# Performance work log

Measured on AMD Instinct MI355X. Metric: run time of the kernel, lower is better.

The kernel has to match this reference:

```python
import jax, jax.numpy as jnp
import numpy as np

N, C, L, D, F = 8, 128, 512, 64, 512
ATTN_W = 64
LN_EPS = 1e-5
ATTN_EPS = 1e-6


def _xavier(k, shape):
    lim = float(np.sqrt(6.0 / (shape[0] + shape[1])))
    return jax.random.uniform(k, shape, jnp.float32, -lim, lim)


def setup_inputs() -> dict:
    key = jax.random.key(0)
    ks = jax.random.split(key, 8)
    return dict(
        x=jax.random.normal(ks[0], (N, C, L), jnp.float32),
        Wx=_xavier(ks[1], (C, D)),
        Wt=_xavier(ks[2], (C, D)),
        bh=jnp.zeros((D,), jnp.float32),
        Wa=_xavier(ks[3], (D, 1)),
        ba=jnp.zeros((1,), jnp.float32),
        W0=_xavier(ks[4], (C, F)),
        b0=jnp.zeros((F,), jnp.float32),
        W1=_xavier(ks[5], (F, C)),
        b1=jnp.zeros((C,), jnp.float32),
        g0=jnp.ones((C,), jnp.float32),
        be0=jnp.zeros((C,), jnp.float32),
        g1=jnp.ones((C,), jnp.float32),
        be1=jnp.zeros((C,), jnp.float32),
    )


def _layernorm(y, g, b):
    mu = jnp.mean(y, axis=-1, keepdims=True)
    var = jnp.var(y, axis=-1, keepdims=True)
    return (y - mu) * jax.lax.rsqrt(var + LN_EPS) * g + b


def reference(x, Wx, Wt, bh, Wa, ba, W0, b0, W1, b1, g0, be0, g1, be1):
    xt = jnp.transpose(x, (0, 2, 1))  # (N, L, C)
    q = jnp.einsum('nlc,cd->nld', xt, Wt)  # (N, L, D)
    k = jnp.einsum('nlc,cd->nld', xt, Wx)  # (N, L, D)
    # additive (Bahdanau) scores: h is the large (N, L, L, D) intermediate
    h = jnp.tanh(q[:, :, None, :] + k[:, None, :, :] + bh)
    e = jnp.einsum('nlmd,d->nlm', h, Wa[:, 0]) + ba[0]  # (N, L, L)
    e = jnp.exp(e - jnp.max(e, axis=-1, keepdims=True))
    # local band mask: tril(w//2 - 1) & triu(-w//2) on (row i, col j)
    dij = jnp.arange(L)[None, :] - jnp.arange(L)[:, None]  # j - i
    mask = (dij <= ATTN_W // 2 - 1) & (dij >= -(ATTN_W // 2))
    e = jnp.where(mask, e, 0.0)
    a = e / (jnp.sum(e, axis=-1, keepdims=True) + ATTN_EPS)  # (N, L, L)
    v = jnp.einsum('nlm,nmc->nlc', a, xt)  # (N, L, C)
    x2 = _layernorm(v + xt, g0, be0)
    x3 = jnp.einsum('nlf,fc->nlc', jax.nn.relu(jnp.einsum('nlc,cf->nlf', x2, W0) + b0), W1) + b1
    x4 = _layernorm(x3 + x2, g1, be1)
    return (jnp.transpose(x4, (0, 2, 1)), a)
```

## Files before the change

### kernel.cpp

```cpp
#include <hip/hip_runtime.h>
#include <hip/hip_fp16.h>
#include <cstddef>


__global__ __launch_bounds__(512) void prep_kernel(
    const float* __restrict__ x, const float* __restrict__ Wt,
    const float* __restrict__ Wx, float* __restrict__ q,
    float* __restrict__ k) {
  __shared__ float xs[128][17];
  int tid = threadIdx.x;
  int n = blockIdx.x >> 5;
  int l0 = (blockIdx.x & 31) << 4;

  {
    int c = tid >> 2, v = tid & 3;
    float4 d4 = *(const float4*)(x + ((size_t)n * 128 + c) * 512 + l0 + 4 * v);
    xs[c][4 * v + 0] = d4.x; xs[c][4 * v + 1] = d4.y;
    xs[c][4 * v + 2] = d4.z; xs[c][4 * v + 3] = d4.w;
  }
  __syncthreads();

  int half = tid >> 8;
  int t = tid & 255;
  int r = t >> 4;
  int f0 = (t & 15) << 2;
  const float* W = half ? Wx : Wt;
  float* dst = half ? k : q;
  float acc[4] = {0.f, 0.f, 0.f, 0.f};
#pragma unroll 4
  for (int cc = 0; cc < 128; cc++) {
    float xv = xs[cc][r];
    float4 w = *(const float4*)(W + cc * 64 + f0);
    acc[0] += xv * w.x; acc[1] += xv * w.y;
    acc[2] += xv * w.z; acc[3] += xv * w.w;
  }
  *(float4*)(dst + ((size_t)n * 512 + l0 + r) * 64 + f0) =
      make_float4(acc[0], acc[1], acc[2], acc[3]);
}

__global__ __launch_bounds__(512, 4) void attn_ffn_fused_kernel(
    const float* __restrict__ x, const float* __restrict__ q,
    const float* __restrict__ k, const float* __restrict__ bh,
    const float* __restrict__ Wa, const float* __restrict__ ba,
    const float* __restrict__ g0, const float* __restrict__ be0,
    const float* __restrict__ W0, const float* __restrict__ b0,
    const float* __restrict__ W1, const float* __restrict__ b1,
    const float* __restrict__ g1, const float* __restrict__ be1,
    float* __restrict__ a, float* __restrict__ out) {
  __shared__ __align__(16) char smem[41328];
  __shared__ __align__(16) float xstT[128][12];
  __shared__ __align__(16) float avT[72][12];
  __shared__ float was[64];

  float (*ks)[68] = (float(*)[68])smem;
  float (*qs)[64] = (float(*)[64])(smem + 19312);
  __half* xtw = (__half*)(smem + 21360);
  float (*partB)[8][128] = (float(*)[8][128])smem;
  float (*tstT)[12] = (float(*)[12])smem;
  float (*part)[8][128] = (float(*)[8][128])smem;

  int tid = threadIdx.x;
  int w = tid >> 6, lane = tid & 63;
  int bid = blockIdx.x;
  int tile = (bid & 7) * 64 + (bid >> 3);
  size_t rbase = (size_t)tile * 8;
  int n = (int)(rbase >> 9);
  int i0 = (int)(rbase & 511);
  int jlo0 = i0 - 32;

  if (tid < 64) was[tid] = Wa[tid];
  for (int idx = tid; idx < 72 * 12; idx += 512) ((float*)avT)[idx] = 0.f;
  if (tid < 128) {
    int r = tid >> 4, d4 = (tid & 15) << 2;
    float4 qv = *(const float4*)(q + ((size_t)n * 512 + i0 + r) * 64 + d4);
    float4 bv = *(const float4*)(bh + d4);
    *(float4*)(&qs[r][d4]) =
        make_float4(qv.x + bv.x, qv.y + bv.y, qv.z + bv.z, qv.w + bv.w);
  }
  for (int idx = tid; idx < 71 * 16; idx += 512) {
    int row = idx >> 4, d4 = (idx & 15) << 2;
    int j = jlo0 + row;
    float4 v = make_float4(0.f, 0.f, 0.f, 0.f);
    if (j >= 0 && j < 512)
      v = *(const float4*)(k + ((size_t)n * 512 + j) * 64 + d4);
    *(float4*)(&ks[row][d4]) = v;
  }
  for (int t = tid; t < 128 * 18; t += 512) {
    int c = t / 18;
    int u = t - c * 18;
    int col = 4 * u;
    int j0 = jlo0 + col;
    const float* xp = x + ((size_t)n * 128 + c) * 512;
    float4 v = make_float4(0.f, 0.f, 0.f, 0.f);
    if (j0 >= 0 && j0 + 3 < 512) {
      v = *(const float4*)(xp + j0);
    } else {
      if (j0 + 0 >= 0 && j0 + 0 < 512) v.x = xp[j0 + 0];
      if (j0 + 1 >= 0 && j0 + 1 < 512) v.y = xp[j0 + 1];
      if (j0 + 2 >= 0 && j0 + 2 < 512) v.z = xp[j0 + 2];
      if (j0 + 3 >= 0 && j0 + 3 < 512) v.w = xp[j0 + 3];
    }
    __half2 p01, p23;
    p01.x = __float2half(v.x); p01.y = __float2half(v.y);
    p23.x = __float2half(v.z); p23.y = __float2half(v.w);
    *(__half2*)(xtw + c * 78 + col) = p01;
    *(__half2*)(xtw + c * 78 + col + 2) = p23;
  }
  __syncthreads();

  {
    int r = w;
    int i = i0 + r;
    int j = jlo0 + r + lane;
    bool valid = (j >= 0 && j < 512);
    const float* krow = &ks[r + lane][0];
    float e = 0.f;
#pragma unroll
    for (int d4 = 0; d4 < 64; d4 += 4) {
      float4 kv = *(const float4*)(krow + d4);
      float4 qv = *(const float4*)(&qs[r][d4]);
      float4 wv = *(const float4*)(&was[d4]);
      float h0 = qv.x + kv.x, h1 = qv.y + kv.y;
      float h2 = qv.z + kv.z, h3 = qv.w + kv.w;
      float t0 = 1.f - 2.f * __builtin_amdgcn_rcpf(__expf(2.f * h0) + 1.f);
      float t1 = 1.f - 2.f * __builtin_amdgcn_rcpf(__expf(2.f * h1) + 1.f);
      float t2 = 1.f - 2.f * __builtin_amdgcn_rcpf(__expf(2.f * h2) + 1.f);
      float t3 = 1.f - 2.f * __builtin_amdgcn_rcpf(__expf(2.f * h3) + 1.f);
      e += wv.x * t0 + wv.y * t1 + wv.z * t2 + wv.w * t3;
    }
    e += ba[0];
    if (!valid) e = -1e30f;

    float m = e;
    for (int o = 32; o > 0; o >>= 1) m = fmaxf(m, __shfl_xor(m, o, 64));
    float ex = valid ? __expf(e - m) : 0.f;
    float s = ex;
    for (int o = 32; o > 0; o >>= 1) s += __shfl_xor(s, o, 64);
    avT[r + lane][r] = ex / (s + 1e-6f);

    float* arow = a + ((size_t)n * 512 + i) * 512;
    int jlo = i - 32;
#pragma unroll
    for (int t = 0; t < 2; t++) {
      int col0 = 4 * lane + 256 * t;
      float4 v;
      { int jr = col0 + 0 - jlo; int jc = min(max(jr, 0), 63); v.x = (jr >= 0 && jr < 64) ? avT[r + jc][r] : 0.f; }
      { int jr = col0 + 1 - jlo; int jc = min(max(jr, 0), 63); v.y = (jr >= 0 && jr < 64) ? avT[r + jc][r] : 0.f; }
      { int jr = col0 + 2 - jlo; int jc = min(max(jr, 0), 63); v.z = (jr >= 0 && jr < 64) ? avT[r + jc][r] : 0.f; }
      { int jr = col0 + 3 - jlo; int jc = min(max(jr, 0), 63); v.w = (jr >= 0 && jr < 64) ? avT[r + jc][r] : 0.f; }
      *(float4*)(arow + col0) = v;
    }
  }
  __syncthreads();

  {
    int c = tid & 127;
    int g = tid >> 7;
    const __half* xr = xtw + c * 78;
    float acc[8] = {0.f, 0.f, 0.f, 0.f, 0.f, 0.f, 0.f, 0.f};
    int colb = 18 * g;
#pragma unroll
    for (int u = 0; u < 9; u++) {
      int col = colb + 2 * u;
      __half2 xh = *(const __half2*)(xr + col);
      float xv0 = __half2float(__low2half(xh));
      float xv1 = __half2float(__high2half(xh));
      float4 a0lo = *(const float4*)(&avT[col][0]);
      float4 a0hi = *(const float4*)(&avT[col][4]);
      float4 a1lo = *(const float4*)(&avT[col + 1][0]);
      float4 a1hi = *(const float4*)(&avT[col + 1][4]);
      acc[0] += a0lo.x * xv0 + a1lo.x * xv1;
      acc[1] += a0lo.y * xv0 + a1lo.y * xv1;
      acc[2] += a0lo.z * xv0 + a1lo.z * xv1;
      acc[3] += a0lo.w * xv0 + a1lo.w * xv1;
      acc[4] += a0hi.x * xv0 + a1hi.x * xv1;
      acc[5] += a0hi.y * xv0 + a1hi.y * xv1;
      acc[6] += a0hi.z * xv0 + a1hi.z * xv1;
      acc[7] += a0hi.w * xv0 + a1hi.w * xv1;
    }
#pragma unroll
    for (int r = 0; r < 8; r++) partB[g][r][c] = acc[r];
  }
  __syncthreads();

  {
    int c = tid & 127;
    int r = tid >> 7;
    const float* xp = x + ((size_t)n * 128 + c) * 512;
    float s0 = partB[0][r][c] + partB[1][r][c] + partB[2][r][c] + partB[3][r][c];
    float s1 = partB[0][r + 4][c] + partB[1][r + 4][c] +
               partB[2][r + 4][c] + partB[3][r + 4][c];
    xstT[c][r] = s0 + xp[i0 + r];
    xstT[c][r + 4] = s1 + xp[i0 + r + 4];
  }
  __syncthreads();

  {
    float a0 = xstT[lane][w], a1 = xstT[lane + 64][w];
    float s = a0 + a1, s2 = a0 * a0 + a1 * a1;
    for (int o = 32; o > 0; o >>= 1) {
      s += __shfl_xor(s, o, 64);
      s2 += __shfl_xor(s2, o, 64);
    }
    float mu = s * (1.f / 128.f);
    float var = s2 * (1.f / 128.f) - mu * mu;
    float rs = rsqrtf(var + 1e-5f);
    xstT[lane][w] = (a0 - mu) * rs * g0[lane] + be0[lane];
    xstT[lane + 64][w] = (a1 - mu) * rs * g0[lane + 64] + be0[lane + 64];
  }
  __syncthreads();

  {
    int g = lane & 15;
    int kq = lane >> 4;
    int f0 = (16 * w + g) << 2;
    int ccb = kq << 5;
    const float* w0p = W0 + (size_t)ccb * 512 + f0;
    float acc[8][4];
#pragma unroll
    for (int i = 0; i < 8; i++)
#pragma unroll
      for (int u = 0; u < 4; u++) acc[i][u] = 0.f;

    float4 wbuf[4];
#pragma unroll
    for (int p = 0; p < 4; p++)
      wbuf[p] = *(const float4*)(w0p + (size_t)p * 512);
#pragma unroll
    for (int c4 = 0; c4 < 8; c4++) {
      float4 cur0 = wbuf[0], cur1 = wbuf[1], cur2 = wbuf[2], cur3 = wbuf[3];
      if (c4 < 7) {
#pragma unroll
        for (int p = 0; p < 4; p++)
          wbuf[p] = *(const float4*)(w0p + (size_t)((c4 + 1) * 4 + p) * 512);
      }
#pragma unroll
      for (int p = 0; p < 4; p++) {
        int cc = ccb + c4 * 4 + p;
        float4 wv = (p == 0) ? cur0 : (p == 1) ? cur1 : (p == 2) ? cur2 : cur3;
        float4 xa = *(const float4*)(&xstT[cc][0]);
        float4 xb = *(const float4*)(&xstT[cc][4]);
        acc[0][0] += xa.x * wv.x; acc[0][1] += xa.x * wv.y; acc[0][2] += xa.x * wv.z; acc[0][3] += xa.x * wv.w;
        acc[1][0] += xa.y * wv.x; acc[1][1] += xa.y * wv.y; acc[1][2] += xa.y * wv.z; acc[1][3] += xa.y * wv.w;
        acc[2][0] += xa.z * wv.x; acc[2][1] += xa.z * wv.y; acc[2][2] += xa.z * wv.z; acc[2][3] += xa.z * wv.w;
        acc[3][0] += xa.w * wv.x; acc[3][1] += xa.w * wv.y; acc[3][2] += xa.w * wv.z; acc[3][3] += xa.w * wv.w;
        acc[4][0] += xb.x * wv.x; acc[4][1] += xb.x * wv.y; acc[4][2] += xb.x * wv.z; acc[4][3] += xb.x * wv.w;
        acc[5][0] += xb.y * wv.x; acc[5][1] += xb.y * wv.y; acc[5][2] += xb.y * wv.z; acc[5][3] += xb.y * wv.w;
        acc[6][0] += xb.z * wv.x; acc[6][1] += xb.z * wv.y; acc[6][2] += xb.z * wv.z; acc[6][3] += xb.z * wv.w;
        acc[7][0] += xb.w * wv.x; acc[7][1] += xb.w * wv.y; acc[7][2] += xb.w * wv.z; acc[7][3] += xb.w * wv.w;
      }
    }
#pragma unroll
    for (int i = 0; i < 8; i++)
#pragma unroll
      for (int u = 0; u < 4; u++) {
        float v = acc[i][u];
        v += __shfl_xor(v, 16, 64);
        v += __shfl_xor(v, 32, 64);
        acc[i][u] = v;
      }
    int f = f0 + kq;
    float bb = b0[f];
    float r0v[8];
#pragma unroll
    for (int i = 0; i < 8; i++) {
      float v = (kq == 0) ? acc[i][0] : (kq == 1) ? acc[i][1]
              : (kq == 2) ? acc[i][2] : acc[i][3];
      r0v[i] = fmaxf(v + bb, 0.f);
    }
    *(float4*)(&tstT[f][0]) = make_float4(r0v[0], r0v[1], r0v[2], r0v[3]);
    *(float4*)(&tstT[f][4]) = make_float4(r0v[4], r0v[5], r0v[6], r0v[7]);
  }
  __syncthreads();

  float g2acc[4][4];
  {
    int c0 = (lane & 31) << 2;
    int rh = lane >> 5;
    const float* W1p = W1 + (size_t)w * 64 * 128 + c0;
    int tb = w << 6;
#pragma unroll
    for (int i = 0; i < 4; i++)
#pragma unroll
      for (int u = 0; u < 4; u++) g2acc[i][u] = 0.f;

    float4 wbuf[4];
#pragma unroll
    for (int p = 0; p < 4; p++)
      wbuf[p] = *(const float4*)(W1p + (size_t)p * 128);
#pragma unroll
    for (int t4 = 0; t4 < 16; t4++) {
      float4 cur0 = wbuf[0], cur1 = wbuf[1], cur2 = wbuf[2], cur3 = wbuf[3];
      if (t4 < 15) {
#pragma unroll
        for (int p = 0; p < 4; p++)
          wbuf[p] = *(const float4*)(W1p + (size_t)((t4 + 1) * 4 + p) * 128);
      }
#pragma unroll
      for (int p = 0; p < 4; p++) {
        int t = t4 * 4 + p;
        float4 wv = (p == 0) ? cur0 : (p == 1) ? cur1 : (p == 2) ? cur2 : cur3;
        float4 tv = *(const float4*)(&tstT[tb + t][4 * rh]);
        g2acc[0][0] += tv.x * wv.x; g2acc[0][1] += tv.x * wv.y; g2acc[0][2] += tv.x * wv.z; g2acc[0][3] += tv.x * wv.w;
        g2acc[1][0] += tv.y * wv.x; g2acc[1][1] += tv.y * wv.y; g2acc[1][2] += tv.y * wv.z; g2acc[1][3] += tv.y * wv.w;
        g2acc[2][0] += tv.z * wv.x; g2acc[2][1] += tv.z * wv.y; g2acc[2][2] += tv.z * wv.z; g2acc[2][3] += tv.z * wv.w;
        g2acc[3][0] += tv.w * wv.x; g2acc[3][1] += tv.w * wv.y; g2acc[3][2] += tv.w * wv.z; g2acc[3][3] += tv.w * wv.w;
      }
    }
  }
  __syncthreads();

  {
    int c0 = (lane & 31) << 2;
    int rh = lane >> 5;
#pragma unroll
    for (int i = 0; i < 4; i++) {
      *(float4*)(&part[w][4 * rh + i][c0]) =
          make_float4(g2acc[i][0], g2acc[i][1], g2acc[i][2], g2acc[i][3]);
    }
  }
  __syncthreads();

  {
    float a0 = b1[lane] + xstT[lane][w];
    float a1 = b1[lane + 64] + xstT[lane + 64][w];
#pragma unroll
    for (int ko = 0; ko < 8; ko++) {
      a0 += part[ko][w][lane];
      a1 += part[ko][w][lane + 64];
    }
    float s = a0 + a1, s2 = a0 * a0 + a1 * a1;
    for (int o = 32; o > 0; o >>= 1) {
      s += __shfl_xor(s, o, 64);
      s2 += __shfl_xor(s2, o, 64);
    }
    float mu = s * (1.f / 128.f);
    float var = s2 * (1.f / 128.f) - mu * mu;
    float rs = rsqrtf(var + 1e-5f);
    xstT[lane][w] = (a0 - mu) * rs * g1[lane] + be1[lane];
    xstT[lane + 64][w] = (a1 - mu) * rs * g1[lane + 64] + be1[lane + 64];
  }
  __syncthreads();

  {
    int c = tid >> 2, tq = tid & 3;
    *(float2*)(out + ((size_t)n * 128 + c) * 512 + i0 + 2 * tq) =
        make_float2(xstT[c][2 * tq], xstT[c][2 * tq + 1]);
  }
}

extern "C" void kernel_launch(void* const* d_in, const int* in_sizes, int n_in,
                              void* d_out, int out_size, void* d_ws, size_t ws_size,
                              hipStream_t stream) {
  const float* x   = (const float*)d_in[0];
  const float* Wx  = (const float*)d_in[1];
  const float* Wt  = (const float*)d_in[2];
  const float* bh  = (const float*)d_in[3];
  const float* Wa  = (const float*)d_in[4];
  const float* ba  = (const float*)d_in[5];
  const float* W0  = (const float*)d_in[6];
  const float* b0  = (const float*)d_in[7];
  const float* W1  = (const float*)d_in[8];
  const float* b1  = (const float*)d_in[9];
  const float* g0  = (const float*)d_in[10];
  const float* be0 = (const float*)d_in[11];
  const float* g1  = (const float*)d_in[12];
  const float* be1 = (const float*)d_in[13];

  float* outx = (float*)d_out;
  float* outa = outx + (size_t)524288;

  float* ws = (float*)d_ws;
  float* q  = ws;
  float* k  = q + 262144;

  prep_kernel<<<256, 512, 0, stream>>>(x, Wt, Wx, q, k);
  attn_ffn_fused_kernel<<<512, 512, 0, stream>>>(
      x, q, k, bh, Wa, ba, g0, be0, W0, b0, W1, b1, g1, be1, outa, outx);
}
```

Baseline: 122.1 us.

## Run FFN matmuls on fp16 MFMA with pre-packed half-precision weights

New measurement: 110.3 us. 1.11x faster.

```diff
diff --git a/kernel.cpp b/kernel.cpp
--- a/kernel.cpp
+++ b/kernel.cpp
@@ -3,10 +3,15 @@
 #include <cstddef>
 
 
+typedef _Float16 half8_t __attribute__((ext_vector_type(8)));
+typedef float f32x4_t __attribute__((ext_vector_type(4)));
+
 __global__ __launch_bounds__(512) void prep_kernel(
     const float* __restrict__ x, const float* __restrict__ Wt,
-    const float* __restrict__ Wx, float* __restrict__ q,
-    float* __restrict__ k) {
+    const float* __restrict__ Wx, const float* __restrict__ W0,
+    const float* __restrict__ W1, float* __restrict__ q,
+    float* __restrict__ k, _Float16* __restrict__ W0p,
+    _Float16* __restrict__ W1p) {
   __shared__ float xs[128][17];
   int tid = threadIdx.x;
   int n = blockIdx.x >> 5;
@@ -36,6 +41,27 @@
   }
   *(float4*)(dst + ((size_t)n * 512 + l0 + r) * 64 + f0) =
       make_float4(acc[0], acc[1], acc[2], acc[3]);
+
+  if (tid < 64) {
+    int b = blockIdx.x;
+    int l15 = tid & 15, lk = tid >> 4;
+    if (b < 128) {
+      int ft = b >> 2, ks = b & 3;
+      const float* src = W0 + (size_t)(ks * 32 + lk * 8) * 512 + ft * 16 + l15;
+      half8_t v;
+#pragma unroll
+      for (int j = 0; j < 8; j++) v[j] = (_Float16)src[(size_t)j * 512];
+      *(half8_t*)(W0p + (size_t)b * 512 + tid * 8) = v;
+    } else {
+      int tt = b - 128;
+      int ft = tt >> 4, ks = tt & 15;
+      const float* src = W1 + (size_t)(ks * 32 + lk * 8) * 128 + ft * 16 + l15;
+      half8_t v;
+#pragma unroll
+      for (int j = 0; j < 8; j++) v[j] = (_Float16)src[(size_t)j * 128];
+      *(half8_t*)(W1p + (size_t)tt * 512 + tid * 8) = v;
+    }
+  }
 }
 
 __global__ __launch_bounds__(512, 4) void attn_ffn_fused_kernel(
@@ -43,8 +69,8 @@
     const float* __restrict__ k, const float* __restrict__ bh,
     const float* __restrict__ Wa, const float* __restrict__ ba,
     const float* __restrict__ g0, const float* __restrict__ be0,
-    const float* __restrict__ W0, const float* __restrict__ b0,
-    const float* __restrict__ W1, const float* __restrict__ b1,
+    const _Float16* __restrict__ W0p, const float* __restrict__ b0,
+    const _Float16* __restrict__ W1p, const float* __restrict__ b1,
     const float* __restrict__ g1, const float* __restrict__ be1,
     float* __restrict__ a, float* __restrict__ out) {
   __shared__ __align__(16) char smem[41328];
@@ -56,8 +82,9 @@
   float (*qs)[64] = (float(*)[64])(smem + 19312);
   __half* xtw = (__half*)(smem + 21360);
   float (*partB)[8][128] = (float(*)[8][128])smem;
-  float (*tstT)[12] = (float(*)[12])smem;
-  float (*part)[8][128] = (float(*)[8][128])smem;
+  _Float16* x2h = (_Float16*)smem;
+  _Float16* tsth = (_Float16*)(smem + 4352);
+  float (*ys)[128] = (float(*)[128])(smem + 20992);
 
   int tid = threadIdx.x;
   int w = tid >> 6, lane = tid & 63;
@@ -211,124 +238,66 @@
   __syncthreads();
 
   {
-    int g = lane & 15;
-    int kq = lane >> 4;
-    int f0 = (16 * w + g) << 2;
-    int ccb = kq << 5;
-    const float* w0p = W0 + (size_t)ccb * 512 + f0;
-    float acc[8][4];
-#pragma unroll
-    for (int i = 0; i < 8; i++)
-#pragma unroll
-      for (int u = 0; u < 4; u++) acc[i][u] = 0.f;
-
-    float4 wbuf[4];
-#pragma unroll
-    for (int p = 0; p < 4; p++)
-      wbuf[p] = *(const float4*)(w0p + (size_t)p * 512);
-#pragma unroll
-    for (int c4 = 0; c4 < 8; c4++) {
-      float4 cur0 = wbuf[0], cur1 = wbuf[1], cur2 = wbuf[2], cur3 = wbuf[3];
-      if (c4 < 7) {
-#pragma unroll
-        for (int p = 0; p < 4; p++)
-          wbuf[p] = *(const float4*)(w0p + (size_t)((c4 + 1) * 4 + p) * 512);
+    half8_t z = {};
+    half8_t* xpad = (half8_t*)(x2h + 8 * 136);
+    for (int idx = tid; idx < 136; idx += 512) xpad[idx] = z;
+    half8_t* tpad = (half8_t*)(tsth + 8 * 520);
+    for (int idx = tid; idx < 520; idx += 512) tpad[idx] = z;
+    int c = tid & 127, rr = tid >> 7;
+    x2h[rr * 136 + c] = (_Float16)xstT[c][rr];
+    x2h[(rr + 4) * 136 + c] = (_Float16)xstT[c][rr + 4];
+  }
+  __syncthreads();
+
+  {
+    int l15 = lane & 15, lk = lane >> 4;
+    const _Float16* arow = x2h + l15 * 136;
+    half8_t afrag[4];
+#pragma unroll
+    for (int ksi = 0; ksi < 4; ksi++)
+      afrag[ksi] = *(const half8_t*)(arow + ksi * 32 + lk * 8);
+#pragma unroll
+    for (int i = 0; i < 4; i++) {
+      int ft = 4 * w + i;
+      f32x4_t acc = {0.f, 0.f, 0.f, 0.f};
+#pragma unroll
+      for (int ksi = 0; ksi < 4; ksi++) {
+        half8_t b = *(const half8_t*)(W0p + ((size_t)(ft * 4 + ksi) << 9) + lane * 8);
+        acc = __builtin_amdgcn_mfma_f32_16x16x32_f16(afrag[ksi], b, acc, 0, 0, 0);
       }
-#pragma unroll
-      for (int p = 0; p < 4; p++) {
-        int cc = ccb + c4 * 4 + p;
-        float4 wv = (p == 0) ? cur0 : (p == 1) ? cur1 : (p == 2) ? cur2 : cur3;
-        float4 xa = *(const float4*)(&xstT[cc][0]);
-        float4 xb = *(const float4*)(&xstT[cc][4]);
-        acc[0][0] += xa.x * wv.x; acc[0][1] += xa.x * wv.y; acc[0][2] += xa.x * wv.z; acc[0][3] += xa.x * wv.w;
-        acc[1][0] += xa.y * wv.x; acc[1][1] += xa.y * wv.y; acc[1][2] += xa.y * wv.z; acc[1][3] += xa.y * wv.w;
-        acc[2][0] += xa.z * wv.x; acc[2][1] += xa.z * wv.y; acc[2][2] += xa.z * wv.z; acc[2][3] += xa.z * wv.w;
-        acc[3][0] += xa.w * wv.x; acc[3][1] += xa.w * wv.y; acc[3][2] += xa.w * wv.z; acc[3][3] += xa.w * wv.w;
-        acc[4][0] += xb.x * wv.x; acc[4][1] += xb.x * wv.y; acc[4][2] += xb.x * wv.z; acc[4][3] += xb.x * wv.w;
-        acc[5][0] += xb.y * wv.x; acc[5][1] += xb.y * wv.y; acc[5][2] += xb.y * wv.z; acc[5][3] += xb.y * wv.w;
-        acc[6][0] += xb.z * wv.x; acc[6][1] += xb.z * wv.y; acc[6][2] += xb.z * wv.z; acc[6][3] += xb.z * wv.w;
-        acc[7][0] += xb.w * wv.x; acc[7][1] += xb.w * wv.y; acc[7][2] += xb.w * wv.z; acc[7][3] += xb.w * wv.w;
+      if (lane < 32) {
+        int fcol = ft * 16 + l15;
+        float bb = b0[fcol];
+        _Float16* tdst = tsth + (lk * 4) * 520 + fcol;
+#pragma unroll
+        for (int j = 0; j < 4; j++)
+          tdst[j * 520] = (_Float16)fmaxf(acc[j] + bb, 0.f);
       }
     }
-#pragma unroll
-    for (int i = 0; i < 8; i++)
-#pragma unroll
-      for (int u = 0; u < 4; u++) {
-        float v = acc[i][u];
-        v += __shfl_xor(v, 16, 64);
-        v += __shfl_xor(v, 32, 64);
-        acc[i][u] = v;
-      }
-    int f = f0 + kq;
-    float bb = b0[f];
-    float r0v[8];
-#pragma unroll
-    for (int i = 0; i < 8; i++) {
-      float v = (kq == 0) ? acc[i][0] : (kq == 1) ? acc[i][1]
-              : (kq == 2) ? acc[i][2] : acc[i][3];
-      r0v[i] = fmaxf(v + bb, 0.f);
-    }
-    *(float4*)(&tstT[f][0]) = make_float4(r0v[0], r0v[1], r0v[2], r0v[3]);
-    *(float4*)(&tstT[f][4]) = make_float4(r0v[4], r0v[5], r0v[6], r0v[7]);
-  }
-  __syncthreads();
-
-  float g2acc[4][4];
-  {
-    int c0 = (lane & 31) << 2;
-    int rh = lane >> 5;
-    const float* W1p = W1 + (size_t)w * 64 * 128 + c0;
-    int tb = w << 6;
-#pragma unroll
-    for (int i = 0; i < 4; i++)
-#pragma unroll
-      for (int u = 0; u < 4; u++) g2acc[i][u] = 0.f;
-
-    float4 wbuf[4];
-#pragma unroll
-    for (int p = 0; p < 4; p++)
-      wbuf[p] = *(const float4*)(W1p + (size_t)p * 128);
-#pragma unroll
-    for (int t4 = 0; t4 < 16; t4++) {
-      float4 cur0 = wbuf[0], cur1 = wbuf[1], cur2 = wbuf[2], cur3 = wbuf[3];
-      if (t4 < 15) {
-#pragma unroll
-        for (int p = 0; p < 4; p++)
-          wbuf[p] = *(const float4*)(W1p + (size_t)((t4 + 1) * 4 + p) * 128);
-      }
-#pragma unroll
-      for (int p = 0; p < 4; p++) {
-        int t = t4 * 4 + p;
-        float4 wv = (p == 0) ? cur0 : (p == 1) ? cur1 : (p == 2) ? cur2 : cur3;
-        float4 tv = *(const float4*)(&tstT[tb + t][4 * rh]);
-        g2acc[0][0] += tv.x * wv.x; g2acc[0][1] += tv.x * wv.y; g2acc[0][2] += tv.x * wv.z; g2acc[0][3] += tv.x * wv.w;
-        g2acc[1][0] += tv.y * wv.x; g2acc[1][1] += tv.y * wv.y; g2acc[1][2] += tv.y * wv.z; g2acc[1][3] += tv.y * wv.w;
-        g2acc[2][0] += tv.z * wv.x; g2acc[2][1] += tv.z * wv.y; g2acc[2][2] += tv.z * wv.z; g2acc[2][3] += tv.z * wv.w;
-        g2acc[3][0] += tv.w * wv.x; g2acc[3][1] += tv.w * wv.y; g2acc[3][2] += tv.w * wv.z; g2acc[3][3] += tv.w * wv.w;
-      }
-    }
-  }
-  __syncthreads();
-
-  {
-    int c0 = (lane & 31) << 2;
-    int rh = lane >> 5;
-#pragma unroll
-    for (int i = 0; i < 4; i++) {
-      *(float4*)(&part[w][4 * rh + i][c0]) =
-          make_float4(g2acc[i][0], g2acc[i][1], g2acc[i][2], g2acc[i][3]);
-    }
-  }
-  __syncthreads();
-
-  {
-    float a0 = b1[lane] + xstT[lane][w];
-    float a1 = b1[lane + 64] + xstT[lane + 64][w];
-#pragma unroll
-    for (int ko = 0; ko < 8; ko++) {
-      a0 += part[ko][w][lane];
-      a1 += part[ko][w][lane + 64];
-    }
+  }
+  __syncthreads();
+
+  {
+    int l15 = lane & 15, lk = lane >> 4;
+    const _Float16* arow = tsth + l15 * 520;
+    f32x4_t acc = {0.f, 0.f, 0.f, 0.f};
+#pragma unroll
+    for (int ksi = 0; ksi < 16; ksi++) {
+      half8_t av = *(const half8_t*)(arow + ksi * 32 + lk * 8);
+      half8_t bv = *(const half8_t*)(W1p + ((size_t)(w * 16 + ksi) << 9) + lane * 8);
+      acc = __builtin_amdgcn_mfma_f32_16x16x32_f16(av, bv, acc, 0, 0, 0);
+    }
+    if (lane < 32) {
+      int c = w * 16 + l15;
+#pragma unroll
+      for (int j = 0; j < 4; j++) ys[lk * 4 + j][c] = acc[j];
+    }
+  }
+  __syncthreads();
+
+  {
+    float a0 = ys[w][lane] + b1[lane] + xstT[lane][w];
+    float a1 = ys[w][lane + 64] + b1[lane + 64] + xstT[lane + 64][w];
     float s = a0 + a1, s2 = a0 * a0 + a1 * a1;
     for (int o = 32; o > 0; o >>= 1) {
       s += __shfl_xor(s, o, 64);
@@ -373,8 +342,10 @@
   float* ws = (float*)d_ws;
   float* q  = ws;
   float* k  = q + 262144;
-
-  prep_kernel<<<256, 512, 0, stream>>>(x, Wt, Wx, q, k);
+  _Float16* W0p = (_Float16*)(k + 262144);
+  _Float16* W1p = W0p + 65536;
+
+  prep_kernel<<<256, 512, 0, stream>>>(x, Wt, Wx, W0, W1, q, k, W0p, W1p);
   attn_ffn_fused_kernel<<<512, 512, 0, stream>>>(
-      x, q, k, bh, Wa, ba, g0, be0, W0, b0, W1, b1, g1, be1, outa, outx);
+      x, q, k, bh, Wa, ba, g0, be0, W0p, b0, W1p, b1, g1, be1, outa, outx);
 }
```
